# Performance work log

Measured on AMD Instinct MI355X. Metric: run time of the kernel, lower is better.

The kernel has to match this reference:

```python
import jax, jax.numpy as jnp
import numpy as np

N, E, H, NH = 10000, 160000, 128, 8
HD = H // NH
LDIM = 8  # (lmax+1)**2 - 1 with lmax=2
CUTOFF = 5.0


def setup_inputs() -> dict:
    key = jax.random.key(0)
    ks = jax.random.split(key, 20)
    w = lambda k, shape: jax.random.normal(k, shape, jnp.float32) * 0.05
    return dict(
        node_feats=jax.random.normal(ks[0], (N, H), jnp.float32),
        edge_feats=jax.random.normal(ks[1], (E, H), jnp.float32),
        vector_feats=jax.random.normal(ks[2], (N, LDIM, H), jnp.float32),
        distances=jax.random.uniform(ks[3], (E,), jnp.float32) * CUTOFF,
        d_ij=jax.random.normal(ks[4], (E, LDIM), jnp.float32),
        senders=jax.random.randint(ks[5], (E,), 0, N),
        receivers=jax.random.randint(ks[6], (E,), 0, N),
        ln_scale=jnp.ones((H,), jnp.float32),
        ln_bias=jnp.zeros((H,), jnp.float32),
        vln_w=jnp.ones((H,), jnp.float32),
        W_vec=w(ks[7], (H, 3 * H)),
        Wq=w(ks[8], (H, H)), bq=jnp.zeros((H,), jnp.float32),
        Wk=w(ks[9], (H, H)), bk=jnp.zeros((H,), jnp.float32),
        Wv=w(ks[10], (H, H)), bv=jnp.zeros((H,), jnp.float32),
        Wdk=w(ks[11], (H, H)), bdk=jnp.zeros((H,), jnp.float32),
        Wdv=w(ks[12], (H, H)), bdv=jnp.zeros((H,), jnp.float32),
        Ws=w(ks[13], (H, 2 * H)), bs=jnp.zeros((2 * H,), jnp.float32),
        Wo=w(ks[14], (H, 3 * H)), bo=jnp.zeros((3 * H,), jnp.float32),
        Wf=w(ks[15], (H, H)), bf=jnp.zeros((H,), jnp.float32),
        Wsrc=w(ks[16], (H, H)),
        Wtrg=w(ks[17], (H, H)),
    )


def _reject(vec, d):
    # vector rejection of vec [E, L, H] against direction d [E, L]
    proj = (vec * d[:, :, None]).sum(axis=1, keepdims=True)
    return vec - proj * d[:, :, None]


def _forward(node_feats, edge_feats, vector_feats, distances, d_ij, senders, receivers,
             ln_scale, ln_bias, vln_w, W_vec, Wq, bq, Wk, bk, Wv, bv, Wdk, bdk, Wdv, bdv,
             Ws, bs, Wo, bo, Wf, bf, Wsrc, Wtrg):
    silu = jax.nn.silu
    n = node_feats.shape[0]
    # LayerNorm (eps=1e-5) on node feats
    mu = node_feats.mean(-1, keepdims=True)
    xc = node_feats - mu
    var = (xc * xc).mean(-1, keepdims=True)
    x = xc * jax.lax.rsqrt(var + 1e-5) * ln_scale + ln_bias
    # VecLayerNorm with norm_type='none' -> identity norm + learned per-channel scale
    vec = vector_feats * vln_w
    q = (x @ Wq + bq).reshape(-1, NH, HD)
    k = (x @ Wk + bk).reshape(-1, NH, HD)
    v = (x @ Wv + bv).reshape(-1, NH, HD)
    dk = silu(edge_feats @ Wdk + bdk).reshape(-1, NH, HD)
    dv = silu(edge_feats @ Wdv + bdv).reshape(-1, NH, HD)
    vec1, vec2, vec3 = jnp.split(vec @ W_vec, [H, 2 * H], axis=-1)
    vec_dot = (vec1 * vec2).sum(axis=1)  # [N, H]
    # per-edge gathers
    q_i = q[receivers]
    k_j = k[senders]
    v_j = v[senders]
    vec_j = vec[senders]  # [E, LDIM, H]
    # attention-style message with cosine cutoff
    cut = 0.5 * (jnp.cos(distances * (jnp.pi / CUTOFF)) + 1.0) * (distances < CUTOFF)
    attn = silu((q_i * k_j * dk).sum(-1)) * cut[:, None]  # [E, NH]
    vj = ((v_j * dv) * attn[:, :, None]).reshape(-1, H)   # [E, H]
    s1, s2 = jnp.split(silu(vj @ Ws + bs), [H], axis=1)
    vec_msg = vec_j * s1[:, None, :] + s2[:, None, :] * d_ij[:, :, None]
    # scatter reduce to nodes
    node_agg = jax.ops.segment_sum(vj, receivers, num_segments=n)
    vec_agg = jax.ops.segment_sum(vec_msg, receivers, num_segments=n)
    o1, o2, o3 = jnp.split(node_agg @ Wo + bo, [H, 2 * H], axis=1)
    dx = vec_dot * o2 + o3
    dvec = vec3 * o1[:, None, :] + vec_agg
    # edge update (last_layer=False)
    w1 = _reject(vec[receivers] @ Wtrg, d_ij)
    w2 = _reject(vec_j @ Wsrc, -d_ij)
    w_dot = (w1 * w2).sum(axis=1)  # [E, H]
    df_ij = silu(edge_feats @ Wf + bf) * w_dot
    return dx, df_ij, dvec


def reference(node_feats, edge_feats, vector_feats, distances, d_ij, senders, receivers,
              ln_scale, ln_bias, vln_w, W_vec, Wq, bq, Wk, bk, Wv, bv, Wdk, bdk, Wdv, bdv,
              Ws, bs, Wo, bo, Wf, bf, Wsrc, Wtrg):
    return _forward(node_feats, edge_feats, vector_feats, distances, d_ij, senders, receivers,
                    ln_scale, ln_bias, vln_w, W_vec, Wq, bq, Wk, bk, Wv, bv, Wdk, bdk, Wdv, bdv,
                    Ws, bs, Wo, bo, Wf, bf, Wsrc, Wtrg)
```

## Files before the change

kernel.cpp:

```cpp
#include <hip/hip_runtime.h>
#include <math.h>

#define NN 10000
#define NE 160000
#define H  128
#define LD 8

typedef unsigned short ushort_t;
typedef short bf16x8 __attribute__((ext_vector_type(8)));
typedef float f32x4 __attribute__((ext_vector_type(4)));

__device__ __forceinline__ float silu_f(float x){ return x / (1.0f + expf(-x)); }
__device__ __forceinline__ float4 f4z(){ return make_float4(0.f,0.f,0.f,0.f); }

__device__ __forceinline__ void fma4(float4& acc, float s, const float4 w){
    acc.x = fmaf(s, w.x, acc.x);
    acc.y = fmaf(s, w.y, acc.y);
    acc.z = fmaf(s, w.z, acc.z);
    acc.w = fmaf(s, w.w, acc.w);
}

__device__ __forceinline__ float4 silu4(float4 a, float4 b){
    return make_float4(silu_f(a.x+b.x), silu_f(a.y+b.y), silu_f(a.z+b.z), silu_f(a.w+b.w));
}

__device__ __forceinline__ ushort_t f2bf(float f){
    union { float f; unsigned int u; } x; x.f = f;
    unsigned int r = x.u + 0x7FFFu + ((x.u >> 16) & 1u);
    return (ushort_t)(r >> 16);
}
__device__ __forceinline__ unsigned int pack2bf(float a, float b){
    return (unsigned int)f2bf(a) | ((unsigned int)f2bf(b) << 16);
}
__device__ __forceinline__ float bf2f_hi(unsigned int u){
    union { unsigned int u; float f; } x; x.u = u & 0xffff0000u; return x.f;
}
__device__ __forceinline__ float bf2f_lo(unsigned int u){
    union { unsigned int u; float f; } x; x.u = u << 16; return x.f;
}

__global__ void k_prepw(const float* __restrict__ Wq, const float* __restrict__ Wk,
                        const float* __restrict__ Wv, const float* __restrict__ W_vec,
                        const float* __restrict__ Wtrg, const float* __restrict__ Wsrc,
                        const float* __restrict__ Wdk, const float* __restrict__ Wdv,
                        const float* __restrict__ Ws,
                        ushort_t* __restrict__ wqkvT, ushort_t* __restrict__ wvecT,
                        ushort_t* __restrict__ wdkT, ushort_t* __restrict__ wdvT,
                        ushort_t* __restrict__ wsT){
    int i = blockIdx.x * 256 + threadIdx.x;
    int n = i >> 7, kk = i & 127;
    if (n < 384){
        float v;
        if (n < 128)      v = Wq[kk*128 + n];
        else if (n < 256) v = Wk[kk*128 + (n-128)];
        else              v = Wv[kk*128 + (n-256)];
        wqkvT[n*128 + kk] = f2bf(v);
    } else if (n < 1024){
        int m = n - 384;
        float v;
        if (m < 384)      v = W_vec[kk*384 + m];
        else if (m < 512) v = Wtrg[kk*128 + (m-384)];
        else              v = Wsrc[kk*128 + (m-512)];
        wvecT[m*128 + kk] = f2bf(v);
    } else if (n < 1152){
        int m = n - 1024;
        wdkT[m*128 + kk] = f2bf(Wdk[kk*128 + m]);
    } else if (n < 1280){
        int m = n - 1152;
        wdvT[m*128 + kk] = f2bf(Wdv[kk*128 + m]);
    } else if (n < 1536){
        int m = n - 1280;
        wsT[m*128 + kk] = f2bf(Ws[kk*256 + m]);
    }
}

__global__ void k_ef2bf(const float* __restrict__ ef, ushort_t* __restrict__ ef_bf){
    size_t i = (size_t)blockIdx.x * 256 + threadIdx.x;
    const float4* s = (const float4*)ef;
    float4 a = s[2*i], b = s[2*i+1];
    uint4 u;
    u.x = pack2bf(a.x, a.y); u.y = pack2bf(a.z, a.w);
    u.z = pack2bf(b.x, b.y); u.w = pack2bf(b.z, b.w);
    ((uint4*)ef_bf)[i] = u;
}

__global__ void k_hist(const int* __restrict__ rcv, int* __restrict__ cnt){
    int e = blockIdx.x * 256 + threadIdx.x;
    if (e < NE) atomicAdd(&cnt[rcv[e]], 1);
}

__global__ __launch_bounds__(256) void k_scan(const int* __restrict__ cnt, int* __restrict__ offs){
    __shared__ int part[256];
    const int t = threadIdx.x;
    const int CH = 40;
    int loc[CH];
    int base = t * CH;
    int lsum = 0;
    if (base < NN){
        #pragma unroll
        for (int i = 0; i < CH; i++){ loc[i] = cnt[base + i]; lsum += loc[i]; }
    }
    part[t] = lsum;
    __syncthreads();
    for (int off = 1; off < 256; off <<= 1){
        int v = (t >= off) ? part[t - off] : 0;
        __syncthreads();
        part[t] += v;
        __syncthreads();
    }
    int ex = part[t] - lsum;
    if (base < NN){
        int run = ex;
        #pragma unroll
        for (int i = 0; i < CH; i++){ offs[base + i] = run; run += loc[i]; }
    }
    if (t == 255) offs[NN] = part[255];
}

__global__ void k_scatter(const int* __restrict__ rcv, const int* __restrict__ offs,
                          int* __restrict__ cnt2, int* __restrict__ eidx){
    int e = blockIdx.x * 256 + threadIdx.x;
    if (e < NE){
        int r = rcv[e];
        int p = atomicAdd(&cnt2[r], 1);
        eidx[offs[r] + p] = e;
    }
}

__global__ __launch_bounds__(128) void node_ln(
    const float* __restrict__ nf, const float* __restrict__ vf,
    const float* __restrict__ ln_s, const float* __restrict__ ln_b,
    const float* __restrict__ vlnw,
    ushort_t* __restrict__ x_bf, ushort_t* __restrict__ vec_bf)
{
    const int n = blockIdx.x, h = threadIdx.x;
    __shared__ float red[4];
    float xv = nf[(size_t)n*H + h];
    float s1 = xv, s2 = xv*xv;
    #pragma unroll
    for (int o = 32; o >= 1; o >>= 1){
        s1 += __shfl_xor(s1, o, 64);
        s2 += __shfl_xor(s2, o, 64);
    }
    const int wid = h >> 6;
    if ((h & 63) == 0){ red[wid] = s1; red[2+wid] = s2; }
    __syncthreads();
    float mean = (red[0] + red[1]) * (1.0f/H);
    float var  = (red[2] + red[3]) * (1.0f/H) - mean*mean;
    float x = (xv - mean) * rsqrtf(var + 1e-5f) * ln_s[h] + ln_b[h];
    x_bf[(size_t)n*H + h] = f2bf(x);
    float w = vlnw[h];
    #pragma unroll
    for (int l = 0; l < LD; l++){
        size_t i = ((size_t)n*LD + l)*H + h;
        vec_bf[i] = f2bf(vf[i] * w);
    }
}

__global__ __launch_bounds__(256) void node_qkv(
    const ushort_t* __restrict__ x_bf, const ushort_t* __restrict__ wqkvT,
    const float* __restrict__ bq, const float* __restrict__ bk, const float* __restrict__ bv,
    float* __restrict__ q, float* __restrict__ k, float* __restrict__ v)
{
    const int tid  = threadIdx.x;
    const int lane = tid & 63;
    const int m0   = (tid >> 6) * 16;
    const int e0   = blockIdx.x * 64;

    const int mrow = lane & 15;
    const int kblk = lane >> 4;

    f32x4 acc[24];
    #pragma unroll
    for (int nt = 0; nt < 24; nt++) acc[nt] = (f32x4)(0.f);

    int arow = e0 + m0 + mrow; if (arow >= NN) arow = NN-1;
    const ushort_t* Arow = x_bf + (size_t)arow*H + kblk*8;
    const ushort_t* wb   = wqkvT + (size_t)mrow*H + kblk*8;

    #pragma unroll
    for (int ks = 0; ks < 4; ks++){
        bf16x8 a = *(const bf16x8*)(Arow + ks*32);
        #pragma unroll
        for (int nt = 0; nt < 24; nt++){
            bf16x8 b8 = *(const bf16x8*)(wb + (size_t)nt*16*H + ks*32);
            acc[nt] = __builtin_amdgcn_mfma_f32_16x16x32_bf16(a, b8, acc[nt], 0, 0, 0);
        }
    }
    float* outs[3] = {q, k, v};
    const float* bias[3] = {bq, bk, bv};
    #pragma unroll
    for (int g = 0; g < 3; g++){
        #pragma unroll
        for (int t = 0; t < 8; t++){
            int col = t*16 + mrow;
            float bb = bias[g][col];
            #pragma unroll
            for (int r = 0; r < 4; r++){
                int row = e0 + m0 + kblk*4 + r;
                if (row < NN) outs[g][(size_t)row*H + col] = acc[g*8+t][r] + bb;
            }
        }
    }
}

__global__ __launch_bounds__(256) void node_vec(
    const ushort_t* __restrict__ vec_bf, const ushort_t* __restrict__ wvecT,
    float* __restrict__ vdot, ushort_t* __restrict__ vec3,
    ushort_t* __restrict__ Vt, ushort_t* __restrict__ Vs)
{
    __shared__ ushort_t st_s[64][136];

    const int tid  = threadIdx.x;
    const int lane = tid & 63;
    const int wv   = tid >> 6;
    const int m0   = wv * 16;
    const size_t r0 = (size_t)blockIdx.x * 64;

    const int mrow = lane & 15;
    const int kblk = lane >> 4;

    f32x4 acc[40];
    #pragma unroll
    for (int nt = 0; nt < 40; nt++) acc[nt] = (f32x4)(0.f);

    const ushort_t* Arow = vec_bf + (r0 + m0 + mrow)*H + kblk*8;
    const ushort_t* wb   = wvecT + (size_t)mrow*H + kblk*8;

    #pragma unroll
    for (int ks = 0; ks < 4; ks++){
        bf16x8 a = *(const bf16x8*)(Arow + ks*32);
        #pragma unroll
        for (int nt = 0; nt < 40; nt++){
            bf16x8 b8 = *(const bf16x8*)(wb + (size_t)nt*16*H + ks*32);
            acc[nt] = __builtin_amdgcn_mfma_f32_16x16x32_bf16(a, b8, acc[nt], 0, 0, 0);
        }
    }

    #pragma unroll
    for (int t = 0; t < 8; t++){
        float p = acc[t][0]*acc[t+8][0] + acc[t][1]*acc[t+8][1]
                + acc[t][2]*acc[t+8][2] + acc[t][3]*acc[t+8][3];
        p += __shfl_xor(p, 16, 64);
        if ((kblk & 1) == 0){
            int node = (int)(r0 >> 3) + wv*2 + (kblk >> 1);
            vdot[(size_t)node*H + t*16 + mrow] = p;
        }
    }

    ushort_t* outs[3] = {vec3, Vt, Vs};
    #pragma unroll
    for (int g = 0; g < 3; g++){
        __syncthreads();
        #pragma unroll
        for (int t = 0; t < 8; t++){
            int coln = t*16 + mrow;
            int lr = m0 + kblk*4;
            st_s[lr+0][coln] = f2bf(acc[16+g*8+t][0]);
            st_s[lr+1][coln] = f2bf(acc[16+g*8+t][1]);
            st_s[lr+2][coln] = f2bf(acc[16+g*8+t][2]);
            st_s[lr+3][coln] = f2bf(acc[16+g*8+t][3]);
        }
        __syncthreads();
        const int rr = tid >> 2, qq = tid & 3;
        uint4* dst = (uint4*)&outs[g][(r0 + rr)*H + qq*32];
        const uint4* src = (const uint4*)&st_s[rr][qq*32];
        dst[0] = src[0]; dst[1] = src[1]; dst[2] = src[2]; dst[3] = src[3];
    }
}

__global__ __launch_bounds__(256) void edge_attn(
    const ushort_t* __restrict__ ef_bf,
    const ushort_t* __restrict__ wdkT, const float* __restrict__ bdk,
    const ushort_t* __restrict__ wdvT, const float* __restrict__ bdv,
    const int* __restrict__ snd, const int* __restrict__ rcv,
    const float* __restrict__ dist,
    const float* __restrict__ q, const float* __restrict__ k, const float* __restrict__ v,
    ushort_t* __restrict__ vj)
{
    __shared__ ushort_t dk_s[64][136];
    __shared__ ushort_t dv_s[64][136];

    const int tid  = threadIdx.x;
    const int lane = tid & 63;
    const int m0   = (tid >> 6) * 16;
    const size_t e0 = (size_t)blockIdx.x * 64;

    const int mrow = lane & 15;
    const int kblk = lane >> 4;

    f32x4 accK[8], accV[8];
    #pragma unroll
    for (int nt = 0; nt < 8; nt++){ accK[nt] = (f32x4)(0.f); accV[nt] = (f32x4)(0.f); }

    const ushort_t* Arow = ef_bf + (e0 + m0 + mrow)*H + kblk*8;
    const ushort_t* wkb  = wdkT + (size_t)mrow*H + kblk*8;
    const ushort_t* wvb  = wdvT + (size_t)mrow*H + kblk*8;

    #pragma unroll
    for (int ks = 0; ks < 4; ks++){
        bf16x8 a = *(const bf16x8*)(Arow + ks*32);
        #pragma unroll
        for (int nt = 0; nt < 8; nt++){
            bf16x8 bk8 = *(const bf16x8*)(wkb + (size_t)nt*16*H + ks*32);
            accK[nt] = __builtin_amdgcn_mfma_f32_16x16x32_bf16(a, bk8, accK[nt], 0, 0, 0);
            bf16x8 bv8 = *(const bf16x8*)(wvb + (size_t)nt*16*H + ks*32);
            accV[nt] = __builtin_amdgcn_mfma_f32_16x16x32_bf16(a, bv8, accV[nt], 0, 0, 0);
        }
    }

    const int lrow = m0 + 4*kblk;
    #pragma unroll
    for (int nt = 0; nt < 8; nt++){
        int coln = nt*16 + mrow;
        float bkn = bdk[coln], bvn = bdv[coln];
        #pragma unroll
        for (int r = 0; r < 4; r++){
            dk_s[lrow + r][coln] = f2bf(silu_f(accK[nt][r] + bkn));
            dv_s[lrow + r][coln] = f2bf(silu_f(accV[nt][r] + bvn));
        }
    }
    __syncthreads();

    const int r  = tid >> 2, cq = tid & 3;
    const size_t e = e0 + r;
    const int s  = snd[e], rr = rcv[e];
    const float d = dist[e];
    const float cut = (d < 5.0f) ? 0.5f*(cosf(d*0.6283185307179586f) + 1.0f) : 0.0f;
    const float* qrow = q + (size_t)rr*H + cq*32;
    const float* krow = k + (size_t)s*H + cq*32;
    const float* vrow = v + (size_t)s*H + cq*32;
    ushort_t* vjrow = vj + e*H + cq*32;

    #pragma unroll
    for (int hh = 0; hh < 2; hh++){
        const int c0 = hh*16;
        float p = 0.f;
        #pragma unroll
        for (int j = 0; j < 4; j++){
            float4 q4 = *(const float4*)(qrow + c0 + 4*j);
            float4 k4 = *(const float4*)(krow + c0 + 4*j);
            uint2 du = *(const uint2*)&dk_s[r][cq*32 + c0 + 4*j];
            p += q4.x*k4.x*bf2f_lo(du.x) + q4.y*k4.y*bf2f_hi(du.x)
               + q4.z*k4.z*bf2f_lo(du.y) + q4.w*k4.w*bf2f_hi(du.y);
        }
        float attn = silu_f(p) * cut;
        #pragma unroll
        for (int j = 0; j < 4; j++){
            float4 v4 = *(const float4*)(vrow + c0 + 4*j);
            uint2 du = *(const uint2*)&dv_s[r][cq*32 + c0 + 4*j];
            uint2 u;
            u.x = pack2bf(v4.x*bf2f_lo(du.x)*attn, v4.y*bf2f_hi(du.x)*attn);
            u.y = pack2bf(v4.z*bf2f_lo(du.y)*attn, v4.w*bf2f_hi(du.y)*attn);
            *(uint2*)(vjrow + c0 + 4*j) = u;
        }
    }
}

__global__ __launch_bounds__(256) void edge_s(
    const ushort_t* __restrict__ vj, const ushort_t* __restrict__ wsT,
    const float* __restrict__ bs, ushort_t* __restrict__ s12)
{
    __shared__ ushort_t s_s[64][264];

    const int tid  = threadIdx.x;
    const int lane = tid & 63;
    const int m0   = (tid >> 6) * 16;
    const size_t e0 = (size_t)blockIdx.x * 64;

    const int mrow = lane & 15;
    const int kblk = lane >> 4;

    f32x4 acc[16];
    #pragma unroll
    for (int nt = 0; nt < 16; nt++) acc[nt] = (f32x4)(0.f);

    const ushort_t* Arow = vj + (e0 + m0 + mrow)*H + kblk*8;
    const ushort_t* wb   = wsT + (size_t)mrow*H + kblk*8;

    #pragma unroll
    for (int ks = 0; ks < 4; ks++){
        bf16x8 a = *(const bf16x8*)(Arow + ks*32);
        #pragma unroll
        for (int nt = 0; nt < 16; nt++){
            bf16x8 b8 = *(const bf16x8*)(wb + (size_t)nt*16*H + ks*32);
            acc[nt] = __builtin_amdgcn_mfma_f32_16x16x32_bf16(a, b8, acc[nt], 0, 0, 0);
        }
    }

    const int lrow = m0 + 4*kblk;
    #pragma unroll
    for (int nt = 0; nt < 16; nt++){
        int coln = nt*16 + mrow;
        float bb = bs[coln];
        #pragma unroll
        for (int r = 0; r < 4; r++)
            s_s[lrow + r][coln] = f2bf(silu_f(acc[nt][r] + bb));
    }
    __syncthreads();

    const int r = tid >> 2, cq = tid & 3;
    const uint4* srcp = (const uint4*)&s_s[r][cq*64];
    uint4* dstp = (uint4*)&s12[(e0 + r)*256 + cq*64];
    #pragma unroll
    for (int j = 0; j < 8; j++) dstp[j] = srcp[j];
}

__global__ __launch_bounds__(256) void edge_df(
    const float* __restrict__ ef, const float* __restrict__ Wf, const float* __restrict__ bf_,
    const int* __restrict__ eidx,
    const int* __restrict__ snd, const int* __restrict__ rcv,
    const float* __restrict__ dij,
    const ushort_t* __restrict__ Vt, const ushort_t* __restrict__ Vs,
    float* __restrict__ df)
{
    __shared__ float wf_s[H][32];
    __shared__ float e_s[32][H+4];
    __shared__ int   eidx_s[32];
    __shared__ int   snd_s[32];
    __shared__ int   rcv_s[32];
    __shared__ float dij_s[32][LD];

    const int tid = threadIdx.x;
    const int by  = blockIdx.y;
    const int p0  = blockIdx.x * 32;

    if (tid < 32) eidx_s[tid] = eidx[p0 + tid];
    __syncthreads();
    if (tid < 32){ int e = eidx_s[tid]; snd_s[tid] = snd[e]; rcv_s[tid] = rcv[e]; }
    for (int i = tid; i < 32*LD; i += 256){
        int row = i >> 3, l = i & 7;
        dij_s[row][l] = dij[(size_t)eidx_s[row]*LD + l];
    }
    for (int i = tid; i < H*8; i += 256){
        int row = i >> 3, c4 = i & 7;
        *(float4*)&wf_s[row][c4*4] = *(const float4*)&Wf[row*H + by*32 + c4*4];
    }
    for (int i = tid; i < 32*32; i += 256){
        int row = i >> 5, c4 = i & 31;
        *(float4*)&e_s[row][c4*4] = *(const float4*)&ef[(size_t)eidx_s[row]*H + c4*4];
    }
    __syncthreads();

    const int g = tid & 7, r0 = tid >> 3;
    float4 af = f4z();
    for (int kk = 0; kk < H; kk++){
        float4 w4 = *(float4*)&wf_s[kk][g*4];
        fma4(af, e_s[r0][kk], w4);
    }
    float4 bf4 = *(const float4*)&bf_[by*32 + g*4];
    float4 f4v = silu4(af, bf4);

    const int e = eidx_s[r0];
    const int s = snd_s[r0], rr = rcv_s[r0];
    const ushort_t* Ar = Vt + (size_t)rr*LD*H + by*32 + g*4;
    const ushort_t* Br = Vs + (size_t)s*LD*H + by*32 + g*4;

    float4 AB = f4z(), aa = f4z(), bb = f4z();
    float dd = 0.f;
    #pragma unroll
    for (int l = 0; l < LD; l++){
        float dl = dij_s[r0][l];
        dd = fmaf(dl, dl, dd);
        uint2 ua = *(const uint2*)&Ar[(size_t)l*H];
        uint2 ub = *(const uint2*)&Br[(size_t)l*H];
        float Ax = bf2f_lo(ua.x), Ay = bf2f_hi(ua.x), Az = bf2f_lo(ua.y), Aw = bf2f_hi(ua.y);
        float Bx = bf2f_lo(ub.x), By = bf2f_hi(ub.x), Bz = bf2f_lo(ub.y), Bw = bf2f_hi(ub.y);
        AB.x = fmaf(Ax, Bx, AB.x); AB.y = fmaf(Ay, By, AB.y);
        AB.z = fmaf(Az, Bz, AB.z); AB.w = fmaf(Aw, Bw, AB.w);
        aa.x = fmaf(Ax, dl, aa.x); aa.y = fmaf(Ay, dl, aa.y);
        aa.z = fmaf(Az, dl, aa.z); aa.w = fmaf(Aw, dl, aa.w);
        bb.x = fmaf(Bx, dl, bb.x); bb.y = fmaf(By, dl, bb.y);
        bb.z = fmaf(Bz, dl, bb.z); bb.w = fmaf(Bw, dl, bb.w);
    }
    float c = 2.0f - dd;
    float4 o = make_float4(f4v.x*(AB.x - aa.x*bb.x*c),
                           f4v.y*(AB.y - aa.y*bb.y*c),
                           f4v.z*(AB.z - aa.z*bb.z*c),
                           f4v.w*(AB.w - aa.w*bb.w*c));
    *(float4*)&df[(size_t)e*H + by*32 + g*4] = o;
}

__global__ __launch_bounds__(256) void node_gather(
    const int* __restrict__ offs, const int* __restrict__ eidx, const int* __restrict__ snd,
    const ushort_t* __restrict__ vj, const ushort_t* __restrict__ s12,
    const float* __restrict__ dij, const ushort_t* __restrict__ vec,
    const float* __restrict__ Wo, const float* __restrict__ bo,
    const float* __restrict__ vdot, const ushort_t* __restrict__ vec3,
    float* __restrict__ dx, float* __restrict__ dvec)
{
    const int n = blockIdx.x;
    const int tid = threadIdx.x;
    const int h = tid & 127;
    const int par = tid >> 7;
    const int beg = offs[n], end = offs[n+1];
    float na = 0.f;
    float av[LD];
    #pragma unroll
    for (int l = 0; l < LD; l++) av[l] = 0.f;

    for (int i = beg + par; i < end; i += 2){
        int e = eidx[i];
        int s = snd[e];
        float vjv = bf2f_lo((unsigned int)vj[(size_t)e*H + h]);
        float s1 = bf2f_lo((unsigned int)s12[(size_t)e*256 + h]);
        float s2 = bf2f_lo((unsigned int)s12[(size_t)e*256 + 128 + h]);
        na += vjv;
        float4 d0 = *(const float4*)&dij[(size_t)e*LD];
        float4 d1 = *(const float4*)&dij[(size_t)e*LD + 4];
        const ushort_t* vr = &vec[(size_t)s*LD*H + h];
        av[0] = fmaf(bf2f_lo((unsigned int)vr[0*H]), s1, fmaf(d0.x, s2, av[0]));
        av[1] = fmaf(bf2f_lo((unsigned int)vr[1*H]), s1, fmaf(d0.y, s2, av[1]));
        av[2] = fmaf(bf2f_lo((unsigned int)vr[2*H]), s1, fmaf(d0.z, s2, av[2]));
        av[3] = fmaf(bf2f_lo((unsigned int)vr[3*H]), s1, fmaf(d0.w, s2, av[3]));
        av[4] = fmaf(bf2f_lo((unsigned int)vr[4*H]), s1, fmaf(d1.x, s2, av[4]));
        av[5] = fmaf(bf2f_lo((unsigned int)vr[5*H]), s1, fmaf(d1.y, s2, av[5]));
        av[6] = fmaf(bf2f_lo((unsigned int)vr[6*H]), s1, fmaf(d1.z, s2, av[6]));
        av[7] = fmaf(bf2f_lo((unsigned int)vr[7*H]), s1, fmaf(d1.w, s2, av[7]));
    }

    __shared__ float red_s[LD+1][128];
    if (par == 0){
        #pragma unroll
        for (int l = 0; l < LD; l++) red_s[l][h] = av[l];
        red_s[LD][h] = na;
    }
    __syncthreads();
    if (par == 1){
        #pragma unroll
        for (int l = 0; l < LD; l++) red_s[l][h] += av[l];
        red_s[LD][h] += na;
    }
    __syncthreads();

    if (par == 0){
        float o1 = bo[h], o2 = bo[H + h], o3 = bo[2*H + h];
        for (int kk = 0; kk < H; kk++){
            float a = red_s[LD][kk];
            o1 = fmaf(a, Wo[kk*(3*H) + h], o1);
            o2 = fmaf(a, Wo[kk*(3*H) + H + h], o2);
            o3 = fmaf(a, Wo[kk*(3*H) + 2*H + h], o3);
        }
        dx[(size_t)n*H + h] = fmaf(vdot[(size_t)n*H + h], o2, o3);
        #pragma unroll
        for (int l = 0; l < LD; l++){
            size_t i2 = ((size_t)n*LD + l)*H + h;
            dvec[i2] = fmaf(bf2f_lo((unsigned int)vec3[i2]), o1, red_s[l][h]);
        }
    }
}

extern "C" void kernel_launch(void* const* d_in, const int* in_sizes, int n_in,
                              void* d_out, int out_size, void* d_ws, size_t ws_size,
                              hipStream_t stream) {
    const float* nf    = (const float*)d_in[0];
    const float* ef    = (const float*)d_in[1];
    const float* vf    = (const float*)d_in[2];
    const float* dist  = (const float*)d_in[3];
    const float* dij   = (const float*)d_in[4];
    const int*   snd   = (const int*)d_in[5];
    const int*   rcv   = (const int*)d_in[6];
    const float* ln_s  = (const float*)d_in[7];
    const float* ln_b  = (const float*)d_in[8];
    const float* vlnw  = (const float*)d_in[9];
    const float* W_vec = (const float*)d_in[10];
    const float* Wq    = (const float*)d_in[11];
    const float* bq    = (const float*)d_in[12];
    const float* Wk    = (const float*)d_in[13];
    const float* bk    = (const float*)d_in[14];
    const float* Wv    = (const float*)d_in[15];
    const float* bv    = (const float*)d_in[16];
    const float* Wdk   = (const float*)d_in[17];
    const float* bdk   = (const float*)d_in[18];
    const float* Wdv   = (const float*)d_in[19];
    const float* bdv   = (const float*)d_in[20];
    const float* Ws    = (const float*)d_in[21];
    const float* bs    = (const float*)d_in[22];
    const float* Wo    = (const float*)d_in[23];
    const float* bo    = (const float*)d_in[24];
    const float* Wf    = (const float*)d_in[25];
    const float* bf_   = (const float*)d_in[26];
    const float* Wsrc  = (const float*)d_in[27];
    const float* Wtrg  = (const float*)d_in[28];

    float* out  = (float*)d_out;
    float* dx   = out;
    float* df   = out + (size_t)NN*H;
    float* dvec = df + (size_t)NE*H;

    float* w = (float*)d_ws;
    size_t off = 0;
    float* q    = w + off; off += (size_t)NN*H;
    float* k    = w + off; off += (size_t)NN*H;
    float* v    = w + off; off += (size_t)NN*H;
    float* vdot = w + off; off += (size_t)NN*H;
    ushort_t* x_bf   = (ushort_t*)(w + off); off += (size_t)NN*H/2;
    ushort_t* vec_bf = (ushort_t*)(w + off); off += (size_t)NN*LD*H/2;
    ushort_t* vec3   = (ushort_t*)(w + off); off += (size_t)NN*LD*H/2;
    ushort_t* Vt     = (ushort_t*)(w + off); off += (size_t)NN*LD*H/2;
    ushort_t* Vs     = (ushort_t*)(w + off); off += (size_t)NN*LD*H/2;
    ushort_t* vj     = (ushort_t*)(w + off); off += (size_t)NE*H/2;
    ushort_t* s12    = (ushort_t*)(w + off); off += (size_t)NE*256/2;
    ushort_t* ef_bf  = s12;
    ushort_t* wqkvT = (ushort_t*)(w + off); off += 384*128/2;
    ushort_t* wvecT = (ushort_t*)(w + off); off += 640*128/2;
    ushort_t* wdkT  = (ushort_t*)(w + off); off += 128*128/2;
    ushort_t* wdvT  = (ushort_t*)(w + off); off += 128*128/2;
    ushort_t* wsT   = (ushort_t*)(w + off); off += 256*128/2;
    int* cnt  = (int*)(w + off); off += NN;
    int* cnt2 = (int*)(w + off); off += NN;
    int* offs = (int*)(w + off); off += NN + 1;
    int* eidx = (int*)(w + off); off += NE;

    hipMemsetAsync(cnt,  0, NN*sizeof(int), stream);
    hipMemsetAsync(cnt2, 0, NN*sizeof(int), stream);

    k_prepw<<<768, 256, 0, stream>>>(Wq, Wk, Wv, W_vec, Wtrg, Wsrc, Wdk, Wdv, Ws,
                                     wqkvT, wvecT, wdkT, wdvT, wsT);
    k_ef2bf<<<NE*H/8/256, 256, 0, stream>>>(ef, ef_bf);

    k_hist<<<(NE+255)/256, 256, 0, stream>>>(rcv, cnt);
    k_scan<<<1, 256, 0, stream>>>(cnt, offs);
    k_scatter<<<(NE+255)/256, 256, 0, stream>>>(rcv, offs, cnt2, eidx);

    node_ln<<<NN, 128, 0, stream>>>(nf, vf, ln_s, ln_b, vlnw, x_bf, vec_bf);

    node_qkv<<<(NN+63)/64, 256, 0, stream>>>(x_bf, wqkvT, bq, bk, bv, q, k, v);

    node_vec<<<NN*LD/64, 256, 0, stream>>>(vec_bf, wvecT, vdot, vec3, Vt, Vs);

    edge_attn<<<NE/64, 256, 0, stream>>>(ef_bf, wdkT, bdk, wdvT, bdv, snd, rcv, dist,
                                         q, k, v, vj);

    edge_df<<<dim3(NE/32, 4), 256, 0, stream>>>(ef, Wf, bf_, eidx, snd, rcv, dij, Vt, Vs, df);

    edge_s<<<NE/64, 256, 0, stream>>>(vj, wsT, bs, s12);

    node_gather<<<NN, 256, 0, stream>>>(offs, eidx, snd, vj, s12, dij, vec_bf,
                                        Wo, bo, vdot, vec3, dx, dvec);
}
```

Baseline: 831.7 us.

## Split edge_df into MFMA edge_f GEMM and separate wdot kernel; widen node_gather

The fp32 scalar edge_feats@Wf GEMM in edge_df is replaced by an MFMA bf16 kernel. It uses a split hi/lo bf16 scheme (four MFMAs per tile) to keep near-fp32 accuracy and writes silu(f) to a scratch buffer aliased onto s12. A separate edge_wdot kernel then does the gather-heavy w_dot product with 64 edges per block and no Wf smem tiling. node_gather moves to 512 threads with 4-way edge partitioning, and the Wo projection is spread across three thread groups. The cost is an extra fp32 E×H round trip through global memory, plus reliance on s12 being consumed or overwritten in order.

```diff
diff --git a/kernel.cpp b/kernel.cpp
--- a/kernel.cpp
+++ b/kernel.cpp
@@ -13,17 +13,6 @@
 __device__ __forceinline__ float silu_f(float x){ return x / (1.0f + expf(-x)); }
 __device__ __forceinline__ float4 f4z(){ return make_float4(0.f,0.f,0.f,0.f); }
 
-__device__ __forceinline__ void fma4(float4& acc, float s, const float4 w){
-    acc.x = fmaf(s, w.x, acc.x);
-    acc.y = fmaf(s, w.y, acc.y);
-    acc.z = fmaf(s, w.z, acc.z);
-    acc.w = fmaf(s, w.w, acc.w);
-}
-
-__device__ __forceinline__ float4 silu4(float4 a, float4 b){
-    return make_float4(silu_f(a.x+b.x), silu_f(a.y+b.y), silu_f(a.z+b.z), silu_f(a.w+b.w));
-}
-
 __device__ __forceinline__ ushort_t f2bf(float f){
     union { float f; unsigned int u; } x; x.f = f;
     unsigned int r = x.u + 0x7FFFu + ((x.u >> 16) & 1u);
@@ -38,15 +27,19 @@
 __device__ __forceinline__ float bf2f_lo(unsigned int u){
     union { unsigned int u; float f; } x; x.u = u << 16; return x.f;
 }
+__device__ __forceinline__ float bfu2f(ushort_t u){
+    union { unsigned int u; float f; } x; x.u = ((unsigned int)u) << 16; return x.f;
+}
 
 __global__ void k_prepw(const float* __restrict__ Wq, const float* __restrict__ Wk,
                         const float* __restrict__ Wv, const float* __restrict__ W_vec,
                         const float* __restrict__ Wtrg, const float* __restrict__ Wsrc,
                         const float* __restrict__ Wdk, const float* __restrict__ Wdv,
-                        const float* __restrict__ Ws,
+                        const float* __restrict__ Ws,  const float* __restrict__ Wf,
                         ushort_t* __restrict__ wqkvT, ushort_t* __restrict__ wvecT,
                         ushort_t* __restrict__ wdkT, ushort_t* __restrict__ wdvT,
-                        ushort_t* __restrict__ wsT){
+                        ushort_t* __restrict__ wsT,
+                        ushort_t* __restrict__ wfT_hi, ushort_t* __restrict__ wfT_lo){
     int i = blockIdx.x * 256 + threadIdx.x;
     int n = i >> 7, kk = i & 127;
     if (n < 384){
@@ -71,6 +64,12 @@
     } else if (n < 1536){
         int m = n - 1280;
         wsT[m*128 + kk] = f2bf(Ws[kk*256 + m]);
+    } else if (n < 1664){
+        int m = n - 1536;
+        float v = Wf[kk*128 + m];
+        ushort_t hi = f2bf(v);
+        wfT_hi[m*128 + kk] = hi;
+        wfT_lo[m*128 + kk] = f2bf(v - bfu2f(hi));
     }
 }
 
@@ -406,82 +405,126 @@
     for (int j = 0; j < 8; j++) dstp[j] = srcp[j];
 }
 
-__global__ __launch_bounds__(256) void edge_df(
-    const float* __restrict__ ef, const float* __restrict__ Wf, const float* __restrict__ bf_,
+__global__ __launch_bounds__(256) void edge_f(
+    const float* __restrict__ ef,
+    const ushort_t* __restrict__ wfT_hi, const ushort_t* __restrict__ wfT_lo,
+    const float* __restrict__ bf_, float* __restrict__ f)
+{
+    const int tid  = threadIdx.x;
+    const int lane = tid & 63;
+    const int m0   = (tid >> 6) * 16;
+    const size_t e0 = (size_t)blockIdx.x * 64;
+
+    const int mrow = lane & 15;
+    const int kblk = lane >> 4;
+
+    f32x4 acc[8];
+    #pragma unroll
+    for (int nt = 0; nt < 8; nt++) acc[nt] = (f32x4)(0.f);
+
+    const float* Arow = ef + (e0 + m0 + mrow)*H + kblk*8;
+    const ushort_t* wh = wfT_hi + (size_t)mrow*H + kblk*8;
+    const ushort_t* wl = wfT_lo + (size_t)mrow*H + kblk*8;
+
+    #pragma unroll
+    for (int ks = 0; ks < 4; ks++){
+        float4 v0 = *(const float4*)(Arow + ks*32);
+        float4 v1 = *(const float4*)(Arow + ks*32 + 4);
+        float vv[8] = {v0.x, v0.y, v0.z, v0.w, v1.x, v1.y, v1.z, v1.w};
+        union { short s[8]; bf16x8 v; } ah, al;
+        #pragma unroll
+        for (int j = 0; j < 8; j++){
+            ushort_t hi = f2bf(vv[j]);
+            ah.s[j] = (short)hi;
+            al.s[j] = (short)f2bf(vv[j] - bfu2f(hi));
+        }
+        #pragma unroll
+        for (int nt = 0; nt < 8; nt++){
+            bf16x8 bh = *(const bf16x8*)(wh + (size_t)nt*16*H + ks*32);
+            bf16x8 bl = *(const bf16x8*)(wl + (size_t)nt*16*H + ks*32);
+            acc[nt] = __builtin_amdgcn_mfma_f32_16x16x32_bf16(ah.v, bh, acc[nt], 0, 0, 0);
+            acc[nt] = __builtin_amdgcn_mfma_f32_16x16x32_bf16(al.v, bh, acc[nt], 0, 0, 0);
+            acc[nt] = __builtin_amdgcn_mfma_f32_16x16x32_bf16(ah.v, bl, acc[nt], 0, 0, 0);
+            acc[nt] = __builtin_amdgcn_mfma_f32_16x16x32_bf16(al.v, bl, acc[nt], 0, 0, 0);
+        }
+    }
+
+    #pragma unroll
+    for (int nt = 0; nt < 8; nt++){
+        int col = nt*16 + mrow;
+        float bb = bf_[col];
+        #pragma unroll
+        for (int r = 0; r < 4; r++)
+            f[(e0 + m0 + 4*kblk + r)*H + col] = silu_f(acc[nt][r] + bb);
+    }
+}
+
+__global__ __launch_bounds__(256) void edge_wdot(
+    const float* __restrict__ f,
     const int* __restrict__ eidx,
     const int* __restrict__ snd, const int* __restrict__ rcv,
     const float* __restrict__ dij,
     const ushort_t* __restrict__ Vt, const ushort_t* __restrict__ Vs,
     float* __restrict__ df)
 {
-    __shared__ float wf_s[H][32];
-    __shared__ float e_s[32][H+4];
-    __shared__ int   eidx_s[32];
-    __shared__ int   snd_s[32];
-    __shared__ int   rcv_s[32];
-    __shared__ float dij_s[32][LD];
+    __shared__ int   eidx_s[64];
+    __shared__ int   snd_s[64];
+    __shared__ int   rcv_s[64];
+    __shared__ float dij_s[64][LD];
 
     const int tid = threadIdx.x;
-    const int by  = blockIdx.y;
-    const int p0  = blockIdx.x * 32;
-
-    if (tid < 32) eidx_s[tid] = eidx[p0 + tid];
-    __syncthreads();
-    if (tid < 32){ int e = eidx_s[tid]; snd_s[tid] = snd[e]; rcv_s[tid] = rcv[e]; }
-    for (int i = tid; i < 32*LD; i += 256){
+    const int p0  = blockIdx.x * 64;
+
+    if (tid < 64) eidx_s[tid] = eidx[p0 + tid];
+    __syncthreads();
+    if (tid < 64){ int e = eidx_s[tid]; snd_s[tid] = snd[e]; rcv_s[tid] = rcv[e]; }
+    for (int i = tid; i < 64*LD; i += 256){
         int row = i >> 3, l = i & 7;
         dij_s[row][l] = dij[(size_t)eidx_s[row]*LD + l];
     }
-    for (int i = tid; i < H*8; i += 256){
-        int row = i >> 3, c4 = i & 7;
-        *(float4*)&wf_s[row][c4*4] = *(const float4*)&Wf[row*H + by*32 + c4*4];
-    }
-    for (int i = tid; i < 32*32; i += 256){
-        int row = i >> 5, c4 = i & 31;
-        *(float4*)&e_s[row][c4*4] = *(const float4*)&ef[(size_t)eidx_s[row]*H + c4*4];
-    }
-    __syncthreads();
-
-    const int g = tid & 7, r0 = tid >> 3;
-    float4 af = f4z();
-    for (int kk = 0; kk < H; kk++){
-        float4 w4 = *(float4*)&wf_s[kk][g*4];
-        fma4(af, e_s[r0][kk], w4);
-    }
-    float4 bf4 = *(const float4*)&bf_[by*32 + g*4];
-    float4 f4v = silu4(af, bf4);
-
-    const int e = eidx_s[r0];
-    const int s = snd_s[r0], rr = rcv_s[r0];
-    const ushort_t* Ar = Vt + (size_t)rr*LD*H + by*32 + g*4;
-    const ushort_t* Br = Vs + (size_t)s*LD*H + by*32 + g*4;
-
-    float4 AB = f4z(), aa = f4z(), bb = f4z();
+    __syncthreads();
+
+    const int r = tid >> 2, cq = tid & 3;
+    const int e = eidx_s[r];
+    const int s = snd_s[r], rr = rcv_s[r];
+    float dl[LD];
     float dd = 0.f;
     #pragma unroll
-    for (int l = 0; l < LD; l++){
-        float dl = dij_s[r0][l];
-        dd = fmaf(dl, dl, dd);
-        uint2 ua = *(const uint2*)&Ar[(size_t)l*H];
-        uint2 ub = *(const uint2*)&Br[(size_t)l*H];
-        float Ax = bf2f_lo(ua.x), Ay = bf2f_hi(ua.x), Az = bf2f_lo(ua.y), Aw = bf2f_hi(ua.y);
-        float Bx = bf2f_lo(ub.x), By = bf2f_hi(ub.x), Bz = bf2f_lo(ub.y), Bw = bf2f_hi(ub.y);
-        AB.x = fmaf(Ax, Bx, AB.x); AB.y = fmaf(Ay, By, AB.y);
-        AB.z = fmaf(Az, Bz, AB.z); AB.w = fmaf(Aw, Bw, AB.w);
-        aa.x = fmaf(Ax, dl, aa.x); aa.y = fmaf(Ay, dl, aa.y);
-        aa.z = fmaf(Az, dl, aa.z); aa.w = fmaf(Aw, dl, aa.w);
-        bb.x = fmaf(Bx, dl, bb.x); bb.y = fmaf(By, dl, bb.y);
-        bb.z = fmaf(Bz, dl, bb.z); bb.w = fmaf(Bw, dl, bb.w);
-    }
-    float c = 2.0f - dd;
-    float4 o = make_float4(f4v.x*(AB.x - aa.x*bb.x*c),
-                           f4v.y*(AB.y - aa.y*bb.y*c),
-                           f4v.z*(AB.z - aa.z*bb.z*c),
-                           f4v.w*(AB.w - aa.w*bb.w*c));
-    *(float4*)&df[(size_t)e*H + by*32 + g*4] = o;
-}
-
-__global__ __launch_bounds__(256) void node_gather(
+    for (int l = 0; l < LD; l++){ dl[l] = dij_s[r][l]; dd = fmaf(dl[l], dl[l], dd); }
+    const float c2 = 2.0f - dd;
+
+    const float*    frow = f  + (size_t)e*H + cq*32;
+    const ushort_t* At   = Vt + (size_t)rr*LD*H + cq*32;
+    const ushort_t* Bs   = Vs + (size_t)s*LD*H + cq*32;
+    float*          dfr  = df + (size_t)e*H + cq*32;
+
+    #pragma unroll
+    for (int cg = 0; cg < 8; cg++){
+        float4 fv = *(const float4*)(frow + cg*4);
+        float4 AB = f4z(), aa = f4z(), bb = f4z();
+        #pragma unroll
+        for (int l = 0; l < LD; l++){
+            float dlv = dl[l];
+            uint2 ua = *(const uint2*)(At + (size_t)l*H + cg*4);
+            uint2 ub = *(const uint2*)(Bs + (size_t)l*H + cg*4);
+            float Ax = bf2f_lo(ua.x), Ay = bf2f_hi(ua.x), Az = bf2f_lo(ua.y), Aw = bf2f_hi(ua.y);
+            float Bx = bf2f_lo(ub.x), By = bf2f_hi(ub.x), Bz = bf2f_lo(ub.y), Bw = bf2f_hi(ub.y);
+            AB.x = fmaf(Ax, Bx, AB.x); AB.y = fmaf(Ay, By, AB.y);
+            AB.z = fmaf(Az, Bz, AB.z); AB.w = fmaf(Aw, Bw, AB.w);
+            aa.x = fmaf(Ax, dlv, aa.x); aa.y = fmaf(Ay, dlv, aa.y);
+            aa.z = fmaf(Az, dlv, aa.z); aa.w = fmaf(Aw, dlv, aa.w);
+            bb.x = fmaf(Bx, dlv, bb.x); bb.y = fmaf(By, dlv, bb.y);
+            bb.z = fmaf(Bz, dlv, bb.z); bb.w = fmaf(Bw, dlv, bb.w);
+        }
+        float4 o = make_float4(fv.x*(AB.x - aa.x*bb.x*c2),
+                               fv.y*(AB.y - aa.y*bb.y*c2),
+                               fv.z*(AB.z - aa.z*bb.z*c2),
+                               fv.w*(AB.w - aa.w*bb.w*c2));
+        *(float4*)(dfr + cg*4) = o;
+    }
+}
+
+__global__ __launch_bounds__(512) void node_gather(
     const int* __restrict__ offs, const int* __restrict__ eidx, const int* __restrict__ snd,
     const ushort_t* __restrict__ vj, const ushort_t* __restrict__ s12,
     const float* __restrict__ dij, const ushort_t* __restrict__ vec,
@@ -499,7 +542,7 @@
     #pragma unroll
     for (int l = 0; l < LD; l++) av[l] = 0.f;
 
-    for (int i = beg + par; i < end; i += 2){
+    for (int i = beg + par; i < end; i += 4){
         int e = eidx[i];
         int s = snd[e];
         float vjv = bf2f_lo((unsigned int)vj[(size_t)e*H + h]);
@@ -519,33 +562,35 @@
         av[7] = fmaf(bf2f_lo((unsigned int)vr[7*H]), s1, fmaf(d1.w, s2, av[7]));
     }
 
-    __shared__ float red_s[LD+1][128];
+    __shared__ float pl[4][LD+1][128];
+    __shared__ float o_s[3][128];
+    #pragma unroll
+    for (int l = 0; l < LD; l++) pl[par][l][h] = av[l];
+    pl[par][LD][h] = na;
+    __syncthreads();
+
     if (par == 0){
         #pragma unroll
-        for (int l = 0; l < LD; l++) red_s[l][h] = av[l];
-        red_s[LD][h] = na;
-    }
-    __syncthreads();
-    if (par == 1){
-        #pragma unroll
-        for (int l = 0; l < LD; l++) red_s[l][h] += av[l];
-        red_s[LD][h] += na;
+        for (int l = 0; l <= LD; l++)
+            pl[0][l][h] = (pl[0][l][h] + pl[1][l][h]) + (pl[2][l][h] + pl[3][l][h]);
+    }
+    __syncthreads();
+
+    if (par > 0){
+        const int g = par - 1;
+        float o = bo[g*H + h];
+        for (int kk = 0; kk < H; kk++)
+            o = fmaf(pl[0][LD][kk], Wo[kk*(3*H) + g*H + h], o);
+        o_s[g][h] = o;
     }
     __syncthreads();
 
     if (par == 0){
-        float o1 = bo[h], o2 = bo[H + h], o3 = bo[2*H + h];
-        for (int kk = 0; kk < H; kk++){
-            float a = red_s[LD][kk];
-            o1 = fmaf(a, Wo[kk*(3*H) + h], o1);
-            o2 = fmaf(a, Wo[kk*(3*H) + H + h], o2);
-            o3 = fmaf(a, Wo[kk*(3*H) + 2*H + h], o3);
-        }
-        dx[(size_t)n*H + h] = fmaf(vdot[(size_t)n*H + h], o2, o3);
+        dx[(size_t)n*H + h] = fmaf(vdot[(size_t)n*H + h], o_s[1][h], o_s[2][h]);
         #pragma unroll
         for (int l = 0; l < LD; l++){
             size_t i2 = ((size_t)n*LD + l)*H + h;
-            dvec[i2] = fmaf(bf2f_lo((unsigned int)vec3[i2]), o1, red_s[l][h]);
+            dvec[i2] = fmaf(bf2f_lo((unsigned int)vec3[i2]), o_s[0][h], pl[0][l][h]);
         }
     }
 }
@@ -602,11 +647,14 @@
     ushort_t* vj     = (ushort_t*)(w + off); off += (size_t)NE*H/2;
     ushort_t* s12    = (ushort_t*)(w + off); off += (size_t)NE*256/2;
     ushort_t* ef_bf  = s12;
-    ushort_t* wqkvT = (ushort_t*)(w + off); off += 384*128/2;
-    ushort_t* wvecT = (ushort_t*)(w + off); off += 640*128/2;
-    ushort_t* wdkT  = (ushort_t*)(w + off); off += 128*128/2;
-    ushort_t* wdvT  = (ushort_t*)(w + off); off += 128*128/2;
-    ushort_t* wsT   = (ushort_t*)(w + off); off += 256*128/2;
+    float*    f      = (float*)s12;
+    ushort_t* wqkvT  = (ushort_t*)(w + off); off += 384*128/2;
+    ushort_t* wvecT  = (ushort_t*)(w + off); off += 640*128/2;
+    ushort_t* wdkT   = (ushort_t*)(w + off); off += 128*128/2;
+    ushort_t* wdvT   = (ushort_t*)(w + off); off += 128*128/2;
+    ushort_t* wsT    = (ushort_t*)(w + off); off += 256*128/2;
+    ushort_t* wfT_hi = (ushort_t*)(w + off); off += 128*128/2;
+    ushort_t* wfT_lo = (ushort_t*)(w + off); off += 128*128/2;
     int* cnt  = (int*)(w + off); off += NN;
     int* cnt2 = (int*)(w + off); off += NN;
     int* offs = (int*)(w + off); off += NN + 1;
@@ -615,8 +663,8 @@
     hipMemsetAsync(cnt,  0, NN*sizeof(int), stream);
     hipMemsetAsync(cnt2, 0, NN*sizeof(int), stream);
 
-    k_prepw<<<768, 256, 0, stream>>>(Wq, Wk, Wv, W_vec, Wtrg, Wsrc, Wdk, Wdv, Ws,
-                                     wqkvT, wvecT, wdkT, wdvT, wsT);
+    k_prepw<<<832, 256, 0, stream>>>(Wq, Wk, Wv, W_vec, Wtrg, Wsrc, Wdk, Wdv, Ws, Wf,
+                                     wqkvT, wvecT, wdkT, wdvT, wsT, wfT_hi, wfT_lo);
     k_ef2bf<<<NE*H/8/256, 256, 0, stream>>>(ef, ef_bf);
 
     k_hist<<<(NE+255)/256, 256, 0, stream>>>(rcv, cnt);
@@ -632,10 +680,12 @@
     edge_attn<<<NE/64, 256, 0, stream>>>(ef_bf, wdkT, bdk, wdvT, bdv, snd, rcv, dist,
                                          q, k, v, vj);
 
-    edge_df<<<dim3(NE/32, 4), 256, 0, stream>>>(ef, Wf, bf_, eidx, snd, rcv, dij, Vt, Vs, df);
+    edge_f<<<NE/64, 256, 0, stream>>>(ef, wfT_hi, wfT_lo, bf_, f);
+
+    edge_wdot<<<NE/64, 256, 0, stream>>>(f, eidx, snd, rcv, dij, Vt, Vs, df);
 
     edge_s<<<NE/64, 256, 0, stream>>>(vj, wsT, bs, s12);
 
-    node_gather<<<NN, 256, 0, stream>>>(offs, eidx, snd, vj, s12, dij, vec_bf,
+    node_gather<<<NN, 512, 0, stream>>>(offs, eidx, snd, vj, s12, dij, vec_bf,
                                         Wo, bo, vdot, vec3, dx, dvec);
 }
```

After: 1.020 ms. 22.7% more time.
